# Performance work log

Hardware: AMD Instinct MI355X
Metric: run time of the kernel (lower is better)

## Reference

```python
import jax, jax.numpy as jnp
import numpy as np

K = 20
EPS = 1e-5

def _knn(x, k):
    # x: (B,C,N); returns indices of k nearest neighbors (incl. self): (B,N,k)
    xx = jnp.sum(x * x, axis=1)                          # (B,N)
    inner = jnp.einsum('bcn,bcm->bnm', x, x)             # (B,N,N)
    neg_d = 2.0 * inner - xx[:, :, None] - xx[:, None, :]
    return jax.lax.top_k(neg_d, k)[1]

def _graph_feature(x, k):
    # x: (B,C,N) -> (B,2C,N,k) with [x_j - x_i, x_i]
    idx = _knn(x, k)
    xt = jnp.transpose(x, (0, 2, 1))                     # (B,N,C)
    nb = jax.vmap(lambda f, i: f[i])(xt, idx)            # (B,N,k,C)
    ctr = xt[:, :, None, :]
    feat = jnp.concatenate([nb - ctr, jnp.broadcast_to(ctr, nb.shape)], axis=-1)
    return jnp.transpose(feat, (0, 3, 1, 2))

def _edge_block(h, w, g, b, k):
    # EdgeConv: graph feature -> 1x1 conv -> BN(eval, mean0/var1) -> LeakyReLU(0.2) -> max over k
    f = _graph_feature(h, k)
    f = jnp.einsum('oc,bcnk->bonk', w, f)
    f = g[None, :, None, None] * f / np.sqrt(1.0 + EPS) + b[None, :, None, None]
    f = jnp.where(f >= 0, f, 0.2 * f)
    return jnp.max(f, axis=-1)                           # (B,O,N)

def _forward(features_1, features_2, sw1, sg1, sb1, fw1, fg1, fb1, sw2, sg2, sb2, fw2, fg2, fb2, sw3, sg3, sb3, fw3, fg3, fb3, ew, eg, eb, att_w, tn_w, tn_wb, tn_bias, fc1_w, fc1_b, sc_w, sc_b):
    def dgcnn_pass(x):
        xyz = x[:, :3, :]
        sem = x[:, 3:, :]
        x1 = _edge_block(xyz, sw1, sg1, sb1, K)
        x2 = _edge_block(x1, sw2, sg2, sb2, K)
        x3 = _edge_block(x2, sw3, sg3, sb3, K)
        s1 = _edge_block(sem, fw1, fg1, fb1, K)
        s2 = _edge_block(s1, fw2, fg2, fb2, K)
        s3 = _edge_block(s2, fw3, fg3, fb3, K)
        h = jnp.concatenate([x3, s3], axis=1)            # (B,2*F3,N)
        h = jnp.einsum('oc,bcn->bon', ew, h)
        h = eg[None, :, None] * h / np.sqrt(1.0 + EPS) + eb[None, :, None]
        h = jnp.where(h >= 0, h, 0.2 * h)
        return jnp.transpose(h, (0, 2, 1))               # (B,N,F3)

    def attention(emb):
        gc = jnp.tanh(jnp.mean(jnp.einsum('bnf,fg->bng', emb, att_w), axis=1))  # (B,F)
        sc = jax.nn.sigmoid(jnp.einsum('bnf,bf->bn', emb, gc))[:, :, None]      # (B,N,1)
        pooled = jnp.einsum('bnf,bnk->bfk', emb, sc)                            # (B,F,1)
        return pooled, sc

    a1 = dgcnn_pass(features_1)
    a2 = dgcnn_pass(features_2)
    p1, att1 = attention(a1)
    p2, att2 = attention(a2)
    e1 = p1[:, :, 0]
    e2 = p2[:, :, 0]
    # NTN: e1^T W[:,:,t] e2 + V [e1;e2] + b
    scoring = jnp.einsum('bf,fgt,bg->bt', e1, tn_w, e2)
    block = jnp.einsum('tc,bc->bt', tn_wb, jnp.concatenate([e1, e2], axis=1))
    tscores = jax.nn.relu(scoring + block + tn_bias[:, 0][None, :])             # (B,T)
    h = jax.nn.relu(tscores @ fc1_w.T + fc1_b)
    score = jax.nn.sigmoid(h @ sc_w.T + sc_b).reshape(-1)                       # (B,)
    return score, att1, att2


def setup_inputs() -> dict:
    key = jax.random.key(0)
    ks = iter(jax.random.split(key, 40))
    def rn(shape, s=0.05):
        return jax.random.normal(next(ks), shape, dtype=jnp.float32) * s
    F1, F2, F3, T, BN = 64, 64, 128, 16, 16
    d = {}
    d['features_1'] = jax.random.normal(next(ks), (8, 131, 1024), dtype=jnp.float32)
    d['features_2'] = jax.random.normal(next(ks), (8, 131, 1024), dtype=jnp.float32)
    d['sw1'] = rn((F1, 6));        d['sg1'] = jnp.ones((F1,));  d['sb1'] = jnp.zeros((F1,))
    d['fw1'] = rn((F1, 256));      d['fg1'] = jnp.ones((F1,));  d['fb1'] = jnp.zeros((F1,))
    d['sw2'] = rn((F2, 2 * F1));   d['sg2'] = jnp.ones((F2,));  d['sb2'] = jnp.zeros((F2,))
    d['fw2'] = rn((F2, 2 * F1));   d['fg2'] = jnp.ones((F2,));  d['fb2'] = jnp.zeros((F2,))
    d['sw3'] = rn((F3, 2 * F2));   d['sg3'] = jnp.ones((F3,));  d['sb3'] = jnp.zeros((F3,))
    d['fw3'] = rn((F3, 2 * F2));   d['fg3'] = jnp.ones((F3,));  d['fb3'] = jnp.zeros((F3,))
    d['ew']  = rn((F3, 2 * F3));   d['eg']  = jnp.ones((F3,));  d['eb']  = jnp.zeros((F3,))
    d['att_w'] = rn((F3, F3))
    d['tn_w'] = rn((F3, F3, T))
    d['tn_wb'] = rn((T, 2 * F3))
    d['tn_bias'] = rn((T, 1))
    d['fc1_w'] = rn((BN, T));  d['fc1_b'] = jnp.zeros((BN,))
    d['sc_w'] = rn((1, BN));   d['sc_b'] = jnp.zeros((1,))
    return d


def reference(features_1, features_2, sw1, sg1, sb1, fw1, fg1, fb1, sw2, sg2, sb2, fw2, fg2, fb2, sw3, sg3, sb3, fw3, fg3, fb3, ew, eg, eb, att_w, tn_w, tn_wb, tn_bias, fc1_w, fc1_b, sc_w, sc_b):
    return _forward(features_1, features_2, sw1, sg1, sb1, fw1, fg1, fb1, sw2, sg2, sb2, fw2, fg2, fb2, sw3, sg3, sb3, fw3, fg3, fb3, ew, eg, eb, att_w, tn_w, tn_wb, tn_bias, fc1_w, fc1_b, sc_w, sc_b)
```

## Files before the change

### kernel.cpp

```cpp
#include <hip/hip_runtime.h>
#include <math.h>

#define INV_SQRT1P 0.99999500003749968754f

typedef short v8s  __attribute__((ext_vector_type(8)));
typedef float v16f __attribute__((ext_vector_type(16)));

static __device__ __forceinline__ float lrelu(float f){ return f >= 0.0f ? f : 0.2f*f; }

static __device__ __forceinline__ int lanecnt_below(unsigned long long m){
  int c = __builtin_amdgcn_mbcnt_lo((unsigned)m, 0u);
  return __builtin_amdgcn_mbcnt_hi((unsigned)(m >> 32), c);
}

__global__ void k_ext3(const float* __restrict__ f1, const float* __restrict__ f2,
                       float* __restrict__ out){
  int i = blockIdx.x*256 + threadIdx.x;
  int half = 8*3*1024;
  if (i >= 2*half) return;
  const float* f = (i < half) ? f1 : f2;
  int boff = (i < half) ? 0 : 8;
  int ii = (i < half) ? i : i - half;
  int n  = ii & 1023;
  int bc = ii >> 10;
  int c  = bc % 3;
  int b  = bc / 3;
  out[((size_t)(((b+boff)<<10)+n))*3 + c] = f[((size_t)(b*131 + c) << 10) + n];
}

__global__ __launch_bounds__(256) void k_extT(const float* __restrict__ f1,
    const float* __restrict__ f2, float* __restrict__ out){
  __shared__ float T[32][65];
  int bid = blockIdx.x;
  int nt = bid & 15;
  int ct = (bid >> 4) & 3;
  int bb = bid >> 6;
  const float* f = (bb < 8) ? f1 : f2;
  int b = bb & 7;
  int tid = threadIdx.x;
  #pragma unroll
  for (int it=0; it<8; it++){
    int cc = it*4 + (tid >> 6);
    int nn = tid & 63;
    T[cc][nn] = f[((size_t)(b*131 + 3 + ct*32 + cc) << 10) + nt*64 + nn];
  }
  __syncthreads();
  size_t rowb = ((size_t)bb << 10) + nt*64;
  #pragma unroll
  for (int it=0; it<8; it++){
    int nn = it*8 + (tid >> 5);
    int c  = tid & 31;
    out[(rowb + nn)*128 + ct*32 + c] = T[c][nn];
  }
}

static __device__ __forceinline__ void pw_body(int bid, int tid,
    const float* __restrict__ X, unsigned short* __restrict__ PH,
    unsigned short* __restrict__ PL, float* __restrict__ xxout,
    const float* __restrict__ Wm, unsigned short* __restrict__ PWH,
    unsigned short* __restrict__ PWL,
    int C, int Kp, int O, int nwblk, int nrowsB, int wsplit, int doxx){
  int nkc = Kp >> 4;
  if (bid < nwblk){
    int gid = bid*256 + tid;
    int nchunk = (nrowsB/32)*nkc;
    if (gid >= nchunk*64) return;
    int lane = gid & 63;
    int chunk = gid >> 6;
    int jb = chunk / nkc, kc = chunk - jb*nkc;
    int j = jb*32 + (lane & 31);
    int k0 = kc*16 + ((lane>>5)<<3);
    unsigned short h[8], lo[8];
    #pragma unroll
    for (int t=0;t<8;t++){
      int k = k0 + t;
      float x = 0.f;
      if (k < C){
        if (wsplit) x = (j < O) ? Wm[(size_t)j*2*C + k] : Wm[(size_t)(j-O)*2*C + C + k];
        else        x = Wm[(size_t)j*C + k];
      }
      unsigned u = __float_as_uint(x);
      unsigned h16 = (u + 0x7fffu + ((u>>16)&1u)) >> 16;
      float hf = __uint_as_float(h16 << 16);
      float lf = x - hf;
      unsigned ul = __float_as_uint(lf);
      unsigned l16 = (ul + 0x7fffu + ((ul>>16)&1u)) >> 16;
      h[t] = (unsigned short)h16; lo[t] = (unsigned short)l16;
    }
    size_t o = (size_t)chunk*512 + lane*8;
    *(v8s*)(PWH + o) = *(v8s*)h;
    *(v8s*)(PWL + o) = *(v8s*)lo;
  } else {
    int gid = (bid - nwblk)*256 + tid;
    int lane = gid & 63;
    int chunk = gid >> 6;
    int rb = chunk / nkc, kc = chunk - rb*nkc;
    int row = rb*32 + (lane & 31);
    int k0 = kc*16 + ((lane>>5)<<3);
    unsigned short h[8], lo[8];
    const float* Xr = X + (size_t)row*C;
    #pragma unroll
    for (int j=0;j<8;j++){
      int k = k0 + j;
      float x = (k < C) ? Xr[k] : 0.f;
      unsigned u = __float_as_uint(x);
      unsigned h16 = (u + 0x7fffu + ((u>>16)&1u)) >> 16;
      float hf = __uint_as_float(h16 << 16);
      float lf = x - hf;
      unsigned ul = __float_as_uint(lf);
      unsigned l16 = (ul + 0x7fffu + ((ul>>16)&1u)) >> 16;
      h[j] = (unsigned short)h16; lo[j] = (unsigned short)l16;
    }
    size_t o = (size_t)chunk*512 + lane*8;
    *(v8s*)(PH + o) = *(v8s*)h;
    *(v8s*)(PL + o) = *(v8s*)lo;
    if (doxx && kc == 0 && (lane & 32) == 0){
      float s = 0.f;
      for (int c=0;c<C;c++) s += Xr[c]*Xr[c];
      xxout[row] = s;
    }
  }
}

__global__ __launch_bounds__(256) void k_pw2(
    const float* __restrict__ XA, unsigned short* __restrict__ PHa,
    unsigned short* __restrict__ PLa, float* __restrict__ xxA,
    const float* __restrict__ WA, unsigned short* __restrict__ PWHa,
    unsigned short* __restrict__ PWLa, int CA, int KpA, int OA, int nwblkA, int nblkA,
    const float* __restrict__ XB, unsigned short* __restrict__ PHb,
    unsigned short* __restrict__ PLb, float* __restrict__ xxB,
    const float* __restrict__ WB, unsigned short* __restrict__ PWHb,
    unsigned short* __restrict__ PWLb, int CB, int KpB, int OB, int nwblkB){
  int bid = blockIdx.x;
  bool isA = bid < nblkA;
  const float* X = isA ? XA : XB;
  unsigned short* PH = isA ? PHa : PHb;
  unsigned short* PL = isA ? PLa : PLb;
  float* xxo = isA ? xxA : xxB;
  const float* Wm = isA ? WA : WB;
  unsigned short* PWH = isA ? PWHa : PWHb;
  unsigned short* PWL = isA ? PWLa : PWLb;
  int C = isA ? CA : CB, Kp = isA ? KpA : KpB, O = isA ? OA : OB;
  int nwblk = isA ? nwblkA : nwblkB;
  int lb = isA ? bid : bid - nblkA;
  pw_body(lb, threadIdx.x, X, PH, PL, xxo, Wm, PWH, PWL, C, Kp, O, nwblk, 2*O, 1, 1);
}

__global__ __launch_bounds__(256) void k_pw(const float* __restrict__ X,
    unsigned short* __restrict__ PH, unsigned short* __restrict__ PL,
    float* __restrict__ xxout, const float* __restrict__ Wm,
    unsigned short* __restrict__ PWH, unsigned short* __restrict__ PWL,
    int C, int Kp, int O, int nwblk, int nrowsB, int wsplit, int doxx){
  pw_body(blockIdx.x, threadIdx.x, X, PH, PL, xxout, Wm, PWH, PWL,
          C, Kp, O, nwblk, nrowsB, wsplit, doxx);
}

static __device__ __forceinline__ void ymf_body(int gw, int l,
    const unsigned short* __restrict__ PH, const unsigned short* __restrict__ PL,
    const unsigned short* __restrict__ PWH, const unsigned short* __restrict__ PWL,
    float* __restrict__ Y, int nkc, int N, int npair){
  int mt = gw / npair;
  int pair = gw - mt*npair;
  int jb0 = pair*2, jb1 = pair*2 + 1;
  size_t ao  = ((size_t)mt*nkc)*512 + l*8;
  size_t b0o = ((size_t)jb0*nkc)*512 + l*8;
  size_t b1o = ((size_t)jb1*nkc)*512 + l*8;
  v16f acc0, acc1;
  #pragma unroll
  for (int i=0;i<16;i++){ acc0[i] = 0.f; acc1[i] = 0.f; }
  for (int kc=0; kc<nkc; kc++){
    v8s Ah  = *(const v8s*)(PH + ao);
    v8s Al  = *(const v8s*)(PL + ao);
    v8s B0h = *(const v8s*)(PWH + b0o);
    v8s B0l = *(const v8s*)(PWL + b0o);
    v8s B1h = *(const v8s*)(PWH + b1o);
    v8s B1l = *(const v8s*)(PWL + b1o);
    acc0 = __builtin_amdgcn_mfma_f32_32x32x16_bf16(Ah, B0h, acc0, 0, 0, 0);
    acc1 = __builtin_amdgcn_mfma_f32_32x32x16_bf16(Ah, B1h, acc1, 0, 0, 0);
    acc0 = __builtin_amdgcn_mfma_f32_32x32x16_bf16(Ah, B0l, acc0, 0, 0, 0);
    acc1 = __builtin_amdgcn_mfma_f32_32x32x16_bf16(Ah, B1l, acc1, 0, 0, 0);
    acc0 = __builtin_amdgcn_mfma_f32_32x32x16_bf16(Al, B0h, acc0, 0, 0, 0);
    acc1 = __builtin_amdgcn_mfma_f32_32x32x16_bf16(Al, B1h, acc1, 0, 0, 0);
    ao += 512; b0o += 512; b1o += 512;
  }
  int rbase = mt*32;
  int c0 = pair*64 + (l & 31), c1 = c0 + 32;
  #pragma unroll
  for (int r=0;r<16;r++){
    int rl_ = (r&3) + ((r>>2)<<3) + ((l>>5)<<2);
    float* dst = Y + (size_t)(rbase + rl_)*N;
    dst[c0] = acc0[r];
    dst[c1] = acc1[r];
  }
}

static __device__ __forceinline__ void dtk_body(float (&Sl)[16][1024], int t, int wave, int l,
    const unsigned short* __restrict__ PH, const unsigned short* __restrict__ PL,
    const float* __restrict__ xx, int* __restrict__ idx, int nkc){
  int rb = ((t & 7) << 6) | (t >> 3);
  int batch = rb >> 5;
  const float* xxb = xx + (batch<<10);
  int rbase_local = (rb & 31)*32;

  v16f acc[4];
  #pragma unroll
  for (int i=0;i<4;i++){
    #pragma unroll
    for (int j=0;j<16;j++) acc[i][j] = 0.f;
  }
  #pragma unroll
  for (int pp=0; pp<2; pp++){
    int pair = wave*2 + pp;
    size_t a   = ((size_t)rb*nkc)*512 + l*8;
    size_t b0o = ((size_t)(batch*32 + 2*pair)*nkc)*512 + l*8;
    size_t b1o = b0o + (size_t)nkc*512;
    for (int kc=0; kc<nkc; kc++){
      v8s Ah  = *(const v8s*)(PH + a);
      v8s Al  = *(const v8s*)(PL + a);
      v8s B0h = *(const v8s*)(PH + b0o);
      v8s B0l = *(const v8s*)(PL + b0o);
      v8s B1h = *(const v8s*)(PH + b1o);
      v8s B1l = *(const v8s*)(PL + b1o);
      acc[2*pp]   = __builtin_amdgcn_mfma_f32_32x32x16_bf16(Ah, B0h, acc[2*pp],   0, 0, 0);
      acc[2*pp+1] = __builtin_amdgcn_mfma_f32_32x32x16_bf16(Ah, B1h, acc[2*pp+1], 0, 0, 0);
      acc[2*pp]   = __builtin_amdgcn_mfma_f32_32x32x16_bf16(Ah, B0l, acc[2*pp],   0, 0, 0);
      acc[2*pp+1] = __builtin_amdgcn_mfma_f32_32x32x16_bf16(Ah, B1l, acc[2*pp+1], 0, 0, 0);
      acc[2*pp]   = __builtin_amdgcn_mfma_f32_32x32x16_bf16(Al, B0h, acc[2*pp],   0, 0, 0);
      acc[2*pp+1] = __builtin_amdgcn_mfma_f32_32x32x16_bf16(Al, B1h, acc[2*pp+1], 0, 0, 0);
      a += 512; b0o += 512; b1o += 512;
    }
  }

  #pragma unroll
  for (int h=0; h<2; h++){
    #pragma unroll
    for (int pp=0; pp<2; pp++){
      int pair = wave*2 + pp;
      int c0 = pair*64 + (l & 31), c1 = c0 + 32;
      float xc0 = xxb[c0], xc1 = xxb[c1];
      #pragma unroll
      for (int r = 0; r < 8; r++){
        int rr = h*8 + r;
        int rl = (rr&3) + (((rr>>2)&1)<<3) + ((l>>5)<<2);
        float xr = xxb[rbase_local + h*16 + rl];
        Sl[rl][c0] = 2.f*acc[2*pp][rr]   - xr - xc0;
        Sl[rl][c1] = 2.f*acc[2*pp+1][rr] - xr - xc1;
      }
    }
    __syncthreads();
    {
      int hi = l >> 5;
      int li = l & 31;
      int rloc = wave*2 + hi;
      int grow = rb*32 + h*16 + rloc;
      int out_base = grow*20;
      unsigned long long hm = hi ? 0xFFFFFFFF00000000ull : 0x00000000FFFFFFFFull;

      unsigned kv[32];
      #pragma unroll
      for (int j=0;j<32;j++){
        unsigned u = __float_as_uint(Sl[rloc][li + 32*j]);
        kv[j] = (u & 0x80000000u) ? ~u : (u | 0x80000000u);
      }

      unsigned lmax = kv[0];
      #pragma unroll
      for (int j=1;j<32;j++) lmax = lmax > kv[j] ? lmax : kv[j];

      unsigned tau = 0u;
      #pragma unroll
      for (int bit=31; bit>=0; --bit){
        unsigned cand = tau | (1u << bit);
        unsigned long long M = __ballot(lmax >= cand);
        int c = hi ? __popc((unsigned)(M >> 32)) : __popc((unsigned)M);
        tau = (c >= 20) ? cand : tau;
      }

      unsigned long long* sl = (unsigned long long*)&Sl[rloc][0];
      sl[li] = 0ull; sl[li+32] = 0ull;
      int b2 = 0;
      #pragma unroll
      for (int j=0;j<32;j++){
        bool p = kv[j] >= tau;
        unsigned long long M = __ballot(p) & hm;
        if (p){
          int s = b2 + lanecnt_below(M);
          if (s < 64) sl[s] = ((unsigned long long)kv[j] << 32) | (unsigned)(li + 32*j);
        }
        b2 += __popcll(M);
      }

      if (b2 <= 64){
        unsigned long long pk0 = sl[li], pk1 = sl[li+32];
        unsigned vcur = 0u;
        #pragma unroll
        for (int bit=31; bit>=0; --bit){
          unsigned long long cc = (unsigned long long)(vcur | (1u << bit)) << 32;
          unsigned long long B0 = __ballot(pk0 >= cc);
          unsigned long long B1 = __ballot(pk1 >= cc);
          int clo = __popc((unsigned)B0) + __popc((unsigned)B1);
          int chi = __popc((unsigned)(B0>>32)) + __popc((unsigned)(B1>>32));
          int c = hi ? chi : clo;
          vcur = (c >= 20) ? (vcur | (1u << bit)) : vcur;
        }
        unsigned k0 = (unsigned)(pk0 >> 32), k1 = (unsigned)(pk1 >> 32);
        unsigned long long G0 = __ballot(k0 > vcur) & hm;
        unsigned long long G1 = __ballot(k1 > vcur) & hm;
        int ng0 = __popcll(G0);
        int c1  = ng0 + __popcll(G1);
        if (k0 > vcur) idx[out_base + lanecnt_below(G0)] = (int)(pk0 & 0xffffffffu);
        if (k1 > vcur) idx[out_base + ng0 + lanecnt_below(G1)] = (int)(pk1 & 0xffffffffu);
        unsigned long long E0 = __ballot(k0 == vcur) & hm;
        unsigned long long E1 = __ballot(k1 == vcur) & hm;
        int ne0 = __popcll(E0);
        if (k0 == vcur){ int s = c1 + lanecnt_below(E0); if (s < 20) idx[out_base + s] = (int)(pk0 & 0xffffffffu); }
        if (k1 == vcur){ int s = c1 + ne0 + lanecnt_below(E1); if (s < 20) idx[out_base + s] = (int)(pk1 & 0xffffffffu); }
      } else {
        unsigned cur = 0u;
        #pragma unroll 1
        for (int bit=31; bit>=0; --bit){
          unsigned cand = cur | (1u << bit);
          int lc = 0;
          #pragma unroll
          for (int j=0;j<32;j++) lc += (kv[j] >= cand) ? 1 : 0;
          #pragma unroll
          for (int off=1; off<32; off<<=1) lc += __shfl_xor(lc, off, 64);
          cur = (lc >= 20) ? cand : cur;
        }
        int bse = 0;
        #pragma unroll 1
        for (int j=0;j<32;j++){
          unsigned long long Mg = __ballot(kv[j] > cur) & hm;
          if (kv[j] > cur){ int s = bse + lanecnt_below(Mg); idx[out_base + s] = li + 32*j; }
          bse += __popcll(Mg);
        }
        #pragma unroll 1
        for (int j=0;j<32;j++){
          unsigned long long Me = __ballot(kv[j] == cur) & hm;
          if (kv[j] == cur){ int s = bse + lanecnt_below(Me); if (s < 20) idx[out_base + s] = li + 32*j; }
          bse += __popcll(Me);
          if (bse >= 20) break;
        }
      }
    }
    __syncthreads();
  }
}

__global__ __launch_bounds__(512) void k_dy2(
    const unsigned short* __restrict__ PHa, const unsigned short* __restrict__ PLa,
    const unsigned short* __restrict__ PWHa, const unsigned short* __restrict__ PWLa,
    const float* __restrict__ xxA, int* __restrict__ idxA, float* __restrict__ Ya,
    int KpA, int NA, int npairA, int nymfA,
    const unsigned short* __restrict__ PHb, const unsigned short* __restrict__ PLb,
    const unsigned short* __restrict__ PWHb, const unsigned short* __restrict__ PWLb,
    const float* __restrict__ xxB, int* __restrict__ idxB, float* __restrict__ Yb,
    int KpB, int NB, int npairB, int nymfB){
  __shared__ float Sl[16][1024];
  int wave = threadIdx.x >> 6;
  int l = threadIdx.x & 63;
  int bid = (int)blockIdx.x;
  int nblkA = nymfA + 512;
  bool isA = bid < nblkA;
  const unsigned short* PH  = isA ? PHa  : PHb;
  const unsigned short* PL  = isA ? PLa  : PLb;
  const unsigned short* PWH = isA ? PWHa : PWHb;
  const unsigned short* PWL = isA ? PWLa : PWLb;
  const float* xx = isA ? xxA : xxB;
  int* idx  = isA ? idxA : idxB;
  float* Y  = isA ? Ya : Yb;
  int Kp    = isA ? KpA : KpB;
  int N     = isA ? NA  : NB;
  int npair = isA ? npairA : npairB;
  int nymf  = isA ? nymfA  : nymfB;
  int lb    = isA ? bid : bid - nblkA;
  if (lb < nymf)
    ymf_body(lb*8 + wave, l, PH, PL, PWH, PWL, Y, Kp >> 4, N, npair);
  else
    dtk_body(Sl, lb - nymf, wave, l, PH, PL, xx, idx, Kp >> 4);
}

__global__ __launch_bounds__(256) void k_emb(const unsigned short* __restrict__ PH,
    const unsigned short* __restrict__ PL, const unsigned short* __restrict__ PWH,
    const unsigned short* __restrict__ PWL, const float* __restrict__ eg,
    const float* __restrict__ eb, float* __restrict__ EMB){
  int w = threadIdx.x >> 6;
  int l = threadIdx.x & 63;
  int gw = blockIdx.x*4 + w;
  int mt = gw >> 1, pair = gw & 1;
  const int nkc = 16;
  size_t ao  = ((size_t)mt*nkc)*512 + l*8;
  size_t b0o = ((size_t)(pair*2)*nkc)*512 + l*8;
  size_t b1o = b0o + (size_t)nkc*512;
  v16f acc0, acc1;
  #pragma unroll
  for (int i=0;i<16;i++){ acc0[i] = 0.f; acc1[i] = 0.f; }
  for (int kc=0; kc<nkc; kc++){
    v8s Ah  = *(const v8s*)(PH + ao);
    v8s Al  = *(const v8s*)(PL + ao);
    v8s B0h = *(const v8s*)(PWH + b0o);
    v8s B0l = *(const v8s*)(PWL + b0o);
    v8s B1h = *(const v8s*)(PWH + b1o);
    v8s B1l = *(const v8s*)(PWL + b1o);
    acc0 = __builtin_amdgcn_mfma_f32_32x32x16_bf16(Ah, B0h, acc0, 0, 0, 0);
    acc1 = __builtin_amdgcn_mfma_f32_32x32x16_bf16(Ah, B1h, acc1, 0, 0, 0);
    acc0 = __builtin_amdgcn_mfma_f32_32x32x16_bf16(Ah, B0l, acc0, 0, 0, 0);
    acc1 = __builtin_amdgcn_mfma_f32_32x32x16_bf16(Ah, B1l, acc1, 0, 0, 0);
    acc0 = __builtin_amdgcn_mfma_f32_32x32x16_bf16(Al, B0h, acc0, 0, 0, 0);
    acc1 = __builtin_amdgcn_mfma_f32_32x32x16_bf16(Al, B1h, acc1, 0, 0, 0);
    ao += 512; b0o += 512; b1o += 512;
  }
  int rbase = mt*32;
  int c0 = pair*64 + (l & 31), c1 = c0 + 32;
  float g0 = eg[c0]*INV_SQRT1P, g1 = eg[c1]*INV_SQRT1P;
  float bb0 = eb[c0], bb1 = eb[c1];
  #pragma unroll
  for (int r=0;r<16;r++){
    int rl_ = (r&3) + ((r>>2)<<3) + ((l>>5)<<2);
    float* dst = EMB + (size_t)(rbase + rl_)*128;
    dst[c0] = lrelu(g0*acc0[r] + bb0);
    dst[c1] = lrelu(g1*acc1[r] + bb1);
  }
}

static __device__ __forceinline__ void edge_body(int bid, int tid, int (&js)[4][20],
    const float* __restrict__ Y, const int* __restrict__ idx,
    const float* __restrict__ g, const float* __restrict__ bias,
    float* __restrict__ out, int O, int ldo, int ooff){
  int rpb = 256/O;
  int rloc = tid/O;
  int o = tid - rloc*O;
  int row = bid*rpb + rloc;
  int b = row >> 10;
  int nj = rpb*20;
  if (tid < nj) js[tid/20][tid%20] = idx[(bid*rpb)*20 + tid];
  __syncthreads();
  int O2 = O*2;
  float y1c = Y[(size_t)row*O2 + o];
  float d   = Y[(size_t)row*O2 + O + o] - y1c;
  float sc  = g[o] * INV_SQRT1P;
  float bb  = bias[o];
  const float* Yb = Y + ((size_t)(b<<10))*O2;
  float best = -1e38f;
  #pragma unroll
  for (int k=0;k<20;k++){
    float f = sc * (Yb[(size_t)js[rloc][k]*O2 + o] + d) + bb;
    best = fmaxf(best, lrelu(f));
  }
  out[(size_t)row*ldo + ooff + o] = best;
}

__global__ __launch_bounds__(256) void k_edge2(
    const float* __restrict__ Ya, const int* __restrict__ idxA,
    const float* __restrict__ gA, const float* __restrict__ bA,
    float* __restrict__ outA, int OA, int ldoA, int ooffA, int ngridA,
    const float* __restrict__ Yb, const int* __restrict__ idxB,
    const float* __restrict__ gB, const float* __restrict__ bB,
    float* __restrict__ outB, int OB, int ldoB, int ooffB){
  __shared__ int js[4][20];
  int bid = (int)blockIdx.x;
  bool isA = bid < ngridA;
  const float* Y = isA ? Ya : Yb;
  const int* idx = isA ? idxA : idxB;
  const float* g = isA ? gA : gB;
  const float* bb = isA ? bA : bB;
  float* o = isA ? outA : outB;
  int O = isA ? OA : OB, ldo = isA ? ldoA : ldoB, ooff = isA ? ooffA : ooffB;
  int lb = isA ? bid : bid - ngridA;
  edge_body(lb, threadIdx.x, js, Y, idx, g, bb, o, O, ldo, ooff);
}

__global__ __launch_bounds__(1024) void k_meangc(const float* __restrict__ emb,
     const float* __restrict__ att_w, float* __restrict__ gc){
  int b = blockIdx.x; int f = threadIdx.x & 127; int ny = threadIdx.x >> 7;
  const float* e = emb + ((size_t)(b<<10) + ny*128)*128 + f;
  float s = 0.f;
  for (int n=0;n<128;n++) s += e[n*128];
  __shared__ float red[8][128];
  __shared__ float mr[128];
  red[ny][f] = s;
  __syncthreads();
  if (ny == 0){
    float t = 0.f;
    #pragma unroll
    for (int i=0;i<8;i++) t += red[i][f];
    mr[f] = t * (1.0f/1024.0f);
  }
  __syncthreads();
  if (threadIdx.x < 128){
    int g = threadIdx.x;
    float s2 = 0.f;
    for (int ff=0; ff<128; ff++) s2 += mr[ff]*att_w[ff*128+g];
    gc[b*128+g] = tanhf(s2);
  }
}

__global__ __launch_bounds__(256) void k_sc(const float* __restrict__ emb, const float* __restrict__ gc,
     float* __restrict__ sc, float* __restrict__ attout){
  int wave = threadIdx.x >> 6;
  int l = threadIdx.x & 63;
  int row = blockIdx.x*4 + wave;
  int b = row >> 10;
  const float* e  = emb + (size_t)row*128;
  const float* gb = gc + b*128;
  float p = e[l]*gb[l] + e[l+64]*gb[l+64];
  #pragma unroll
  for (int off=32; off>0; off>>=1) p += __shfl_xor(p, off, 64);
  if (l == 0){
    float s = 1.0f/(1.0f + expf(-p));
    sc[row] = s;
    attout[row] = s;
  }
}

__global__ __launch_bounds__(1024) void k_pool(const float* __restrict__ emb, const float* __restrict__ sc,
     float* __restrict__ ep){
  int b = blockIdx.x; int f = threadIdx.x & 127; int ny = threadIdx.x >> 7;
  const float* e  = emb + ((size_t)(b<<10) + ny*128)*128 + f;
  const float* sb = sc + (b<<10) + ny*128;
  float s = 0.f;
  for (int n=0;n<128;n++) s += e[n*128]*sb[n];
  __shared__ float red[8][128];
  red[ny][f] = s;
  __syncthreads();
  if (ny == 0){
    float t = 0.f;
    #pragma unroll
    for (int i=0;i<8;i++) t += red[i][f];
    ep[b*128+f] = t;
  }
}

__global__ __launch_bounds__(256) void k_tnet(const float* __restrict__ e1, const float* __restrict__ e2,
    const float* __restrict__ tn_w, const float* __restrict__ tn_wb, const float* __restrict__ tn_bias,
    float* __restrict__ tsout){
  int b = blockIdx.x; int t = threadIdx.x; int tt = t & 15; int fs = t >> 4;
  __shared__ float E1[128], E2[128], red[16][17];
  if (t < 128){ E1[t] = e1[b*128+t]; E2[t] = e2[b*128+t]; }
  __syncthreads();
  float acc = 0.f;
  for (int f = fs*8; f < fs*8+8; f++){
    const float* tw = tn_w + f*128*16 + tt;
    float partial = 0.f;
    for (int g=0; g<128; g++) partial += E2[g]*tw[g*16];
    acc += E1[f]*partial;
  }
  red[fs][tt] = acc;
  __syncthreads();
  if (t < 16){
    float s = 0.f;
    #pragma unroll
    for (int i=0;i<16;i++) s += red[i][t];
    float acc2 = 0.f;
    for (int c=0;c<128;c++) acc2 += tn_wb[t*256+c]*E1[c] + tn_wb[t*256+128+c]*E2[c];
    float v = s + acc2 + tn_bias[t];
    tsout[b*16+t] = v > 0.f ? v : 0.f;
  }
}

__global__ __launch_bounds__(128) void k_score2(const float* __restrict__ ts,
   const float* __restrict__ fc1_w, const float* __restrict__ fc1_b,
   const float* __restrict__ sc_w, const float* __restrict__ sc_b, float* __restrict__ out){
  int t = threadIdx.x; int b = t >> 4, i = t & 15;
  __shared__ float h2[8][17];
  float a = 0.f;
  #pragma unroll
  for (int k=0;k<16;k++) a += ts[b*16+k]*fc1_w[i*16+k];
  a += fc1_b[i];
  h2[b][i] = a > 0.f ? a : 0.f;
  __syncthreads();
  if (t < 8){
    float s = 0.f;
    #pragma unroll
    for (int k=0;k<16;k++) s += h2[t][k]*sc_w[k];
    s += sc_b[0];
    out[t] = 1.0f/(1.0f + expf(-s));
  }
}

extern "C" void kernel_launch(void* const* d_in, const int* in_sizes, int n_in,
                              void* d_out, int out_size, void* d_ws, size_t ws_size,
                              hipStream_t stream){
  const float* f1  = (const float*)d_in[0];
  const float* f2  = (const float*)d_in[1];
  const float* sw1 = (const float*)d_in[2];  const float* sg1 = (const float*)d_in[3];  const float* sb1 = (const float*)d_in[4];
  const float* fw1 = (const float*)d_in[5];  const float* fg1 = (const float*)d_in[6];  const float* fb1 = (const float*)d_in[7];
  const float* sw2 = (const float*)d_in[8];  const float* sg2 = (const float*)d_in[9];  const float* sb2 = (const float*)d_in[10];
  const float* fw2 = (const float*)d_in[11]; const float* fg2 = (const float*)d_in[12]; const float* fb2 = (const float*)d_in[13];
  const float* sw3 = (const float*)d_in[14]; const float* sg3 = (const float*)d_in[15]; const float* sb3 = (const float*)d_in[16];
  const float* fw3 = (const float*)d_in[17]; const float* fg3 = (const float*)d_in[18]; const float* fb3 = (const float*)d_in[19];
  const float* ew  = (const float*)d_in[20]; const float* eg  = (const float*)d_in[21]; const float* eb  = (const float*)d_in[22];
  const float* att_w   = (const float*)d_in[23];
  const float* tn_w    = (const float*)d_in[24];
  const float* tn_wb   = (const float*)d_in[25];
  const float* tn_bias = (const float*)d_in[26];
  const float* fc1_w   = (const float*)d_in[27];
  const float* fc1_b   = (const float*)d_in[28];
  const float* sc_w    = (const float*)d_in[29];
  const float* sc_b    = (const float*)d_in[30];

  float* W    = (float*)d_ws;
  float* Tx0  = W;
  float* Tx1  = W + 1048576;
  float* Ts0  = W + 2097152;
  float* Ts1  = W + 4194304;
  float* X3S3 = W + 5242880;
  float* EMB  = W + 9437184;
  float* xxA  = W + 11534336;
  float* xxB  = W + 11550720;
  float* gcb  = W + 11567104;
  float* scb  = W + 11569152;
  float* ep   = W + 11585536;
  float* tsb  = W + 11587584;
  int*   idxA = (int*)(W + 11587712);
  int*   idxB = (int*)(W + 11915392);
  unsigned short* PHa  = (unsigned short*)(W + 12243072);
  unsigned short* PLa  = (unsigned short*)(W + 13291648);
  unsigned short* PHb  = (unsigned short*)(W + 14340224);
  unsigned short* PLb  = (unsigned short*)(W + 15388800);
  unsigned short* PWHa = (unsigned short*)(W + 16437376);
  unsigned short* PWLa = (unsigned short*)(W + 16453760);
  unsigned short* PWHb = (unsigned short*)(W + 16470144);
  unsigned short* PWLb = (unsigned short*)(W + 16486528);
  float* REGa = W + 16502912;
  float* REGb = W + 20697216;
  unsigned short* PH2 = (unsigned short*)(W + 24891520);
  unsigned short* PL2 = (unsigned short*)(W + 26988672);

  (void)ws_size;
  float* out = (float*)d_out;

  auto edge2 = [&](const float* xa, int CA, int OA, const float* wa,
                   const float* ga, const float* ba, float* xoutA, int ldoA, int ooffA,
                   const float* xb, int CB, int OB, const float* wb,
                   const float* gb, const float* bb, float* xoutB, int ldoB, int ooffB){
    int KpA = (CA + 15) & ~15, KpB = (CB + 15) & ~15;
    int nkcA = KpA >> 4,       nkcB = KpB >> 4;
    int npairA = 2*OA/64,      npairB = 2*OB/64;
    int nwblkA = ((2*OA/32)*nkcA*64 + 255)/256;
    int nwblkB = ((2*OB/32)*nkcB*64 + 255)/256;
    int nblkA  = nwblkA + 128*nkcA;
    int nblkB  = nwblkB + 128*nkcB;
    int nymfA  = 64*npairA, nymfB = 64*npairB;
    k_pw2<<<nblkA + nblkB, 256, 0, stream>>>(
        xa, PHa, PLa, xxA, wa, PWHa, PWLa, CA, KpA, OA, nwblkA, nblkA,
        xb, PHb, PLb, xxB, wb, PWHb, PWLb, CB, KpB, OB, nwblkB);
    k_dy2<<<(nymfA + 512) + (nymfB + 512), 512, 0, stream>>>(
        PHa, PLa, PWHa, PWLa, xxA, idxA, REGa, KpA, 2*OA, npairA, nymfA,
        PHb, PLb, PWHb, PWLb, xxB, idxB, REGb, KpB, 2*OB, npairB, nymfB);
    int ngridA = 16384/(256/OA);
    int ngridB = 16384/(256/OB);
    k_edge2<<<ngridA + ngridB, 256, 0, stream>>>(
        REGa, idxA, ga, ba, xoutA, OA, ldoA, ooffA, ngridA,
        REGb, idxB, gb, bb, xoutB, OB, ldoB, ooffB);
  };

  k_ext3<<<(2*8*3*1024+255)/256, 256, 0, stream>>>(f1, f2, Tx0);
  k_extT<<<1024, 256, 0, stream>>>(f1, f2, Ts0);
  edge2(Tx0, 3,   64, sw1, sg1, sb1, Tx1, 64, 0,
        Ts0, 128, 64, fw1, fg1, fb1, Ts1, 64, 0);
  edge2(Tx1, 64,  64, sw2, sg2, sb2, Tx0, 64, 0,
        Ts1, 64,  64, fw2, fg2, fb2, Ts0, 64, 0);
  edge2(Tx0, 64, 128, sw3, sg3, sb3, X3S3, 256, 0,
        Ts0, 64, 128, fw3, fg3, fb3, X3S3, 256, 128);
  {
    int nwblk = ((128/32)*16*64 + 255)/256;
    k_pw<<<nwblk + 128*16, 256, 0, stream>>>(X3S3, PH2, PL2, xxA, ew, PWHa, PWLa,
        256, 256, 128, nwblk, 128, 0, 0);
    k_emb<<<256, 256, 0, stream>>>(PH2, PL2, PWHa, PWLa, eg, eb, EMB);
  }
  k_meangc<<<16, 1024, 0, stream>>>(EMB, att_w, gcb);
  k_sc<<<4096, 256, 0, stream>>>(EMB, gcb, scb, out + 8);
  k_pool<<<16, 1024, 0, stream>>>(EMB, scb, ep);

  k_tnet<<<8, 256, 0, stream>>>(ep, ep + 1024, tn_w, tn_wb, tn_bias, tsb);
  k_score2<<<1, 128, 0, stream>>>(tsb, fc1_w, fc1_b, sc_w, sc_b, out);
}
```

Before: 455.3 us.

## Fuse edge max-pool epilogue with next layer's bf16 split packing and weight prep

Replaces the separate edge kernel plus the next layer's pointwise pack kernel with one k_ep2 kernel. It computes the EdgeConv max over neighbours, the squared norm for the next kNN, and writes the hi/lo bf16 MFMA-packed activations directly from shared memory, while extra blocks pack the next layer's weights. This removes the fp32 intermediate write/read round trips and several kernel launches per layer. The cost is more shared-memory syncs per block and only 32 threads doing the packing stores.

```diff
diff --git a/kernel.cpp b/kernel.cpp
--- a/kernel.cpp
+++ b/kernel.cpp
@@ -144,15 +144,6 @@
   int nwblk = isA ? nwblkA : nwblkB;
   int lb = isA ? bid : bid - nblkA;
   pw_body(lb, threadIdx.x, X, PH, PL, xxo, Wm, PWH, PWL, C, Kp, O, nwblk, 2*O, 1, 1);
-}
-
-__global__ __launch_bounds__(256) void k_pw(const float* __restrict__ X,
-    unsigned short* __restrict__ PH, unsigned short* __restrict__ PL,
-    float* __restrict__ xxout, const float* __restrict__ Wm,
-    unsigned short* __restrict__ PWH, unsigned short* __restrict__ PWL,
-    int C, int Kp, int O, int nwblk, int nrowsB, int wsplit, int doxx){
-  pw_body(blockIdx.x, threadIdx.x, X, PH, PL, xxout, Wm, PWH, PWL,
-          C, Kp, O, nwblk, nrowsB, wsplit, doxx);
 }
 
 static __device__ __forceinline__ void ymf_body(int gw, int l,
@@ -380,6 +371,110 @@
     dtk_body(Sl, lb - nymf, wave, l, PH, PL, xx, idx, Kp >> 4);
 }
 
+static __device__ __forceinline__ void ep_body(int bid, int tid,
+    float (&Bsh)[512], int (&js)[4][20],
+    const float* __restrict__ Y, const int* __restrict__ idx,
+    const float* __restrict__ g, const float* __restrict__ bias,
+    unsigned short* __restrict__ PH, unsigned short* __restrict__ PL,
+    float* __restrict__ xxout, int O, int kcoff, int nkcT, int doxx){
+  int rpb = 256/O;
+  int rloc = tid/O;
+  int o = tid - rloc*O;
+  int row0 = bid*rpb;
+  int row = row0 + rloc;
+  int b = row >> 10;
+  if (tid < rpb*20) js[tid/20][tid%20] = idx[row0*20 + tid];
+  __syncthreads();
+  int O2 = O*2;
+  float y1c = Y[(size_t)row*O2 + o];
+  float d   = Y[(size_t)row*O2 + O + o] - y1c;
+  float sc  = g[o] * INV_SQRT1P;
+  float bb  = bias[o];
+  const float* Yb = Y + ((size_t)(b<<10))*O2;
+  float best = -1e38f;
+  #pragma unroll
+  for (int k=0;k<20;k++){
+    float f = sc * (Yb[(size_t)js[rloc][k]*O2 + o] + d) + bb;
+    best = fmaxf(best, lrelu(f));
+  }
+  Bsh[rloc*O + o] = best;
+  __syncthreads();
+  int wave = tid >> 6, l = tid & 63;
+  if (doxx && wave < rpb){
+    float s = 0.f;
+    for (int t=l; t<O; t+=64){ float v = Bsh[wave*O + t]; s += v*v; }
+    #pragma unroll
+    for (int off=32; off>0; off>>=1) s += __shfl_xor(s, off, 64);
+    if (l == 0) xxout[row0 + wave] = s;
+  }
+  if (tid < 32){
+    int perrow = (O >> 4)*2;
+    int r2 = tid / perrow, pos = tid - r2*perrow;
+    int kcl = pos >> 1, half = pos & 1;
+    int row2 = row0 + r2, rb32 = row2 >> 5, lr = row2 & 31;
+    int k0 = kcl*16 + half*8;
+    unsigned short h[8], lo8[8];
+    #pragma unroll
+    for (int j=0;j<8;j++){
+      float x = Bsh[r2*O + k0 + j];
+      unsigned u = __float_as_uint(x);
+      unsigned h16 = (u + 0x7fffu + ((u>>16)&1u)) >> 16;
+      float hf = __uint_as_float(h16 << 16);
+      float lf = x - hf;
+      unsigned ul = __float_as_uint(lf);
+      unsigned l16 = (ul + 0x7fffu + ((ul>>16)&1u)) >> 16;
+      h[j] = (unsigned short)h16; lo8[j] = (unsigned short)l16;
+    }
+    size_t off = ((size_t)(rb32*nkcT + kcoff + kcl))*512 + (half*32 + lr)*8;
+    *(v8s*)(PH + off) = *(v8s*)h;
+    *(v8s*)(PL + off) = *(v8s*)lo8;
+  }
+}
+
+__global__ __launch_bounds__(256) void k_ep2(
+    const float* __restrict__ WmA, unsigned short* __restrict__ PWHa2,
+    unsigned short* __restrict__ PWLa2, int CwA, int KpwA, int OwA, int wsA, int nrA, int nwA,
+    const float* __restrict__ WmB, unsigned short* __restrict__ PWHb2,
+    unsigned short* __restrict__ PWLb2, int CwB, int KpwB, int OwB, int wsB, int nrB, int nwB,
+    const float* __restrict__ Ya, const int* __restrict__ idxA,
+    const float* __restrict__ gA, const float* __restrict__ bA,
+    unsigned short* __restrict__ PHa2, unsigned short* __restrict__ PLa2,
+    float* __restrict__ xxA2, int OA, int kcoffA, int nkcA, int doxxA, int ngeA,
+    const float* __restrict__ Yb, const int* __restrict__ idxB,
+    const float* __restrict__ gB, const float* __restrict__ bB,
+    unsigned short* __restrict__ PHb2, unsigned short* __restrict__ PLb2,
+    float* __restrict__ xxB2, int OB, int kcoffB, int nkcB, int doxxB){
+  __shared__ float Bsh[512];
+  __shared__ int js[4][20];
+  int bid = (int)blockIdx.x, tid = threadIdx.x;
+  int nw = nwA + nwB;
+  if (bid < nw){
+    bool isA = bid < nwA;
+    const float* Wm = isA ? WmA : WmB;
+    unsigned short* PWH = isA ? PWHa2 : PWHb2;
+    unsigned short* PWL = isA ? PWLa2 : PWLb2;
+    int C = isA ? CwA : CwB, Kp = isA ? KpwA : KpwB, O = isA ? OwA : OwB;
+    int ws = isA ? wsA : wsB, nr = isA ? nrA : nrB;
+    int lb = isA ? bid : bid - nwA;
+    pw_body(lb, tid, (const float*)0, (unsigned short*)0, (unsigned short*)0,
+            (float*)0, Wm, PWH, PWL, C, Kp, O, 1<<30, nr, ws, 0);
+  } else {
+    int eb = bid - nw;
+    bool isA = eb < ngeA;
+    const float* Y = isA ? Ya : Yb;
+    const int* idx = isA ? idxA : idxB;
+    const float* g = isA ? gA : gB;
+    const float* bi = isA ? bA : bB;
+    unsigned short* PH = isA ? PHa2 : PHb2;
+    unsigned short* PL = isA ? PLa2 : PLb2;
+    float* xxo = isA ? xxA2 : xxB2;
+    int O = isA ? OA : OB, kcoff = isA ? kcoffA : kcoffB;
+    int nkcT = isA ? nkcA : nkcB, doxx = isA ? doxxA : doxxB;
+    int lb = isA ? eb : eb - ngeA;
+    ep_body(lb, tid, Bsh, js, Y, idx, g, bi, PH, PL, xxo, O, kcoff, nkcT, doxx);
+  }
+}
+
 __global__ __launch_bounds__(256) void k_emb(const unsigned short* __restrict__ PH,
     const unsigned short* __restrict__ PL, const unsigned short* __restrict__ PWH,
     const unsigned short* __restrict__ PWL, const float* __restrict__ eg,
@@ -421,53 +516,6 @@
     dst[c0] = lrelu(g0*acc0[r] + bb0);
     dst[c1] = lrelu(g1*acc1[r] + bb1);
   }
-}
-
-static __device__ __forceinline__ void edge_body(int bid, int tid, int (&js)[4][20],
-    const float* __restrict__ Y, const int* __restrict__ idx,
-    const float* __restrict__ g, const float* __restrict__ bias,
-    float* __restrict__ out, int O, int ldo, int ooff){
-  int rpb = 256/O;
-  int rloc = tid/O;
-  int o = tid - rloc*O;
-  int row = bid*rpb + rloc;
-  int b = row >> 10;
-  int nj = rpb*20;
-  if (tid < nj) js[tid/20][tid%20] = idx[(bid*rpb)*20 + tid];
-  __syncthreads();
-  int O2 = O*2;
-  float y1c = Y[(size_t)row*O2 + o];
-  float d   = Y[(size_t)row*O2 + O + o] - y1c;
-  float sc  = g[o] * INV_SQRT1P;
-  float bb  = bias[o];
-  const float* Yb = Y + ((size_t)(b<<10))*O2;
-  float best = -1e38f;
-  #pragma unroll
-  for (int k=0;k<20;k++){
-    float f = sc * (Yb[(size_t)js[rloc][k]*O2 + o] + d) + bb;
-    best = fmaxf(best, lrelu(f));
-  }
-  out[(size_t)row*ldo + ooff + o] = best;
-}
-
-__global__ __launch_bounds__(256) void k_edge2(
-    const float* __restrict__ Ya, const int* __restrict__ idxA,
-    const float* __restrict__ gA, const float* __restrict__ bA,
-    float* __restrict__ outA, int OA, int ldoA, int ooffA, int ngridA,
-    const float* __restrict__ Yb, const int* __restrict__ idxB,
-    const float* __restrict__ gB, const float* __restrict__ bB,
-    float* __restrict__ outB, int OB, int ldoB, int ooffB){
-  __shared__ int js[4][20];
-  int bid = (int)blockIdx.x;
-  bool isA = bid < ngridA;
-  const float* Y = isA ? Ya : Yb;
-  const int* idx = isA ? idxA : idxB;
-  const float* g = isA ? gA : gB;
-  const float* bb = isA ? bA : bB;
-  float* o = isA ? outA : outB;
-  int O = isA ? OA : OB, ldo = isA ? ldoA : ldoB, ooff = isA ? ooffA : ooffB;
-  int lb = isA ? bid : bid - ngridA;
-  edge_body(lb, threadIdx.x, js, Y, idx, g, bb, o, O, ldo, ooff);
 }
 
 __global__ __launch_bounds__(1024) void k_meangc(const float* __restrict__ emb,
@@ -601,10 +649,7 @@
 
   float* W    = (float*)d_ws;
   float* Tx0  = W;
-  float* Tx1  = W + 1048576;
   float* Ts0  = W + 2097152;
-  float* Ts1  = W + 4194304;
-  float* X3S3 = W + 5242880;
   float* EMB  = W + 9437184;
   float* xxA  = W + 11534336;
   float* xxB  = W + 11550720;
@@ -630,45 +675,43 @@
   (void)ws_size;
   float* out = (float*)d_out;
 
-  auto edge2 = [&](const float* xa, int CA, int OA, const float* wa,
-                   const float* ga, const float* ba, float* xoutA, int ldoA, int ooffA,
-                   const float* xb, int CB, int OB, const float* wb,
-                   const float* gb, const float* bb, float* xoutB, int ldoB, int ooffB){
-    int KpA = (CA + 15) & ~15, KpB = (CB + 15) & ~15;
-    int nkcA = KpA >> 4,       nkcB = KpB >> 4;
-    int npairA = 2*OA/64,      npairB = 2*OB/64;
-    int nwblkA = ((2*OA/32)*nkcA*64 + 255)/256;
-    int nwblkB = ((2*OB/32)*nkcB*64 + 255)/256;
-    int nblkA  = nwblkA + 128*nkcA;
-    int nblkB  = nwblkB + 128*nkcB;
-    int nymfA  = 64*npairA, nymfB = 64*npairB;
-    k_pw2<<<nblkA + nblkB, 256, 0, stream>>>(
-        xa, PHa, PLa, xxA, wa, PWHa, PWLa, CA, KpA, OA, nwblkA, nblkA,
-        xb, PHb, PLb, xxB, wb, PWHb, PWLb, CB, KpB, OB, nwblkB);
-    k_dy2<<<(nymfA + 512) + (nymfB + 512), 512, 0, stream>>>(
-        PHa, PLa, PWHa, PWLa, xxA, idxA, REGa, KpA, 2*OA, npairA, nymfA,
-        PHb, PLb, PWHb, PWLb, xxB, idxB, REGb, KpB, 2*OB, npairB, nymfB);
-    int ngridA = 16384/(256/OA);
-    int ngridB = 16384/(256/OB);
-    k_edge2<<<ngridA + ngridB, 256, 0, stream>>>(
-        REGa, idxA, ga, ba, xoutA, OA, ldoA, ooffA, ngridA,
-        REGb, idxB, gb, bb, xoutB, OB, ldoB, ooffB);
-  };
-
   k_ext3<<<(2*8*3*1024+255)/256, 256, 0, stream>>>(f1, f2, Tx0);
   k_extT<<<1024, 256, 0, stream>>>(f1, f2, Ts0);
-  edge2(Tx0, 3,   64, sw1, sg1, sb1, Tx1, 64, 0,
-        Ts0, 128, 64, fw1, fg1, fb1, Ts1, 64, 0);
-  edge2(Tx1, 64,  64, sw2, sg2, sb2, Tx0, 64, 0,
-        Ts1, 64,  64, fw2, fg2, fb2, Ts0, 64, 0);
-  edge2(Tx0, 64, 128, sw3, sg3, sb3, X3S3, 256, 0,
-        Ts0, 64, 128, fw3, fg3, fb3, X3S3, 256, 128);
+
   {
-    int nwblk = ((128/32)*16*64 + 255)/256;
-    k_pw<<<nwblk + 128*16, 256, 0, stream>>>(X3S3, PH2, PL2, xxA, ew, PWHa, PWLa,
-        256, 256, 128, nwblk, 128, 0, 0);
-    k_emb<<<256, 256, 0, stream>>>(PH2, PL2, PWHa, PWLa, eg, eb, EMB);
-  }
+    int nwblkA = ((2*64/32)*1*64 + 255)/256;
+    int nwblkB = ((2*64/32)*8*64 + 255)/256;
+    int nblkA  = nwblkA + 128*1;
+    int nblkB  = nwblkB + 128*8;
+    k_pw2<<<nblkA + nblkB, 256, 0, stream>>>(
+        Tx0, PHa, PLa, xxA, sw1, PWHa, PWLa, 3, 16, 64, nwblkA, nblkA,
+        Ts0, PHb, PLb, xxB, fw1, PWHb, PWLb, 128, 128, 64, nwblkB);
+    k_dy2<<<(128+512)+(128+512), 512, 0, stream>>>(
+        PHa, PLa, PWHa, PWLa, xxA, idxA, REGa, 16, 128, 2, 128,
+        PHb, PLb, PWHb, PWLb, xxB, idxB, REGb, 128, 128, 2, 128);
+  }
+  k_ep2<<<4+4+4096+4096, 256, 0, stream>>>(
+      sw2, PWHa, PWLa, 64, 64, 64, 1, 128, 4,
+      fw2, PWHb, PWLb, 64, 64, 64, 1, 128, 4,
+      REGa, idxA, sg1, sb1, PHa, PLa, xxA, 64, 0, 4, 1, 4096,
+      REGb, idxB, fg1, fb1, PHb, PLb, xxB, 64, 0, 4, 1);
+  k_dy2<<<(128+512)+(128+512), 512, 0, stream>>>(
+      PHa, PLa, PWHa, PWLa, xxA, idxA, REGa, 64, 128, 2, 128,
+      PHb, PLb, PWHb, PWLb, xxB, idxB, REGb, 64, 128, 2, 128);
+  k_ep2<<<8+8+4096+4096, 256, 0, stream>>>(
+      sw3, PWHa, PWLa, 64, 64, 128, 1, 256, 8,
+      fw3, PWHb, PWLb, 64, 64, 128, 1, 256, 8,
+      REGa, idxA, sg2, sb2, PHa, PLa, xxA, 64, 0, 4, 1, 4096,
+      REGb, idxB, fg2, fb2, PHb, PLb, xxB, 64, 0, 4, 1);
+  k_dy2<<<(256+512)+(256+512), 512, 0, stream>>>(
+      PHa, PLa, PWHa, PWLa, xxA, idxA, REGa, 64, 256, 4, 256,
+      PHb, PLb, PWHb, PWLb, xxB, idxB, REGb, 64, 256, 4, 256);
+  k_ep2<<<16+0+8192+8192, 256, 0, stream>>>(
+      ew, PWHa, PWLa, 256, 256, 128, 0, 128, 16,
+      ew, PWHb, PWLb, 256, 256, 128, 0, 128, 0,
+      REGa, idxA, sg3, sb3, PH2, PL2, xxA, 128, 0, 16, 0, 8192,
+      REGb, idxB, fg3, fb3, PH2, PL2, xxB, 128, 8, 16, 0);
+  k_emb<<<256, 256, 0, stream>>>(PH2, PL2, PWHa, PWLa, eg, eb, EMB);
   k_meangc<<<16, 1024, 0, stream>>>(EMB, att_w, gcb);
   k_sc<<<4096, 256, 0, stream>>>(EMB, gcb, scb, out + 8);
   k_pool<<<16, 1024, 0, stream>>>(EMB, scb, ep);
```

Measured after the change: 436.4 us, median of 2. 4.1% less time.
